# Performance work log

Measured on AMD Instinct MI355X. Metric: run time of the kernel, lower is better.

## Reference

```python
import jax, jax.numpy as jnp
import numpy as np

TEMPERATURE = 2.0 / 3.0
LIMIT_A = -0.1
LIMIT_B = 1.1

N_NODES = 50000
N_CLUSTERS = 64
N_RELATIONS = 8
N_EDGES = 1000000


def setup_inputs() -> dict:
    key = jax.random.key(0)
    ks = jax.random.split(key, 6)
    xavier = float(np.sqrt(6.0 / (N_CLUSTERS + N_CLUSTERS)))
    return {
        "assignments": jax.random.normal(ks[0], (N_NODES, N_CLUSTERS), jnp.float32),
        "inter_cluster_logits": jax.random.uniform(ks[1], (N_RELATIONS, N_CLUSTERS, N_CLUSTERS), jnp.float32, -xavier, xavier),
        "log_alpha": jnp.zeros((N_RELATIONS, N_CLUSTERS, N_CLUSTERS), jnp.float32),
        "absent_bias": jnp.zeros((N_RELATIONS,), jnp.float32),
        "edge_index": jax.random.randint(ks[2], (2, N_EDGES), 0, N_NODES, jnp.int32),
        "edge_type": jax.random.randint(ks[3], (N_EDGES,), 0, N_RELATIONS, jnp.int32),
        "neg_edge_index": jax.random.randint(ks[4], (2, N_EDGES), 0, N_NODES, jnp.int32),
        "neg_edge_type": jax.random.randint(ks[5], (N_EDGES,), 0, N_RELATIONS, jnp.int32),
    }


def _edge_logits(assignments, weights, absent_bias, edge_index, edge_type):
    # src, dst: [E, C] gathers (irregular access)
    src = assignments[edge_index[0]]
    dst = assignments[edge_index[1]]
    n_rel = weights.shape[0]
    # torch.bmm(W[et], dst[:, :, None]) == dst @ W[et].T ; compute per relation
    # (fixed small relation loop; avoids materializing [E, C, C]) then select.
    logits_all = jnp.stack(
        [jnp.sum(src * (dst @ weights[r].T), axis=-1) for r in range(n_rel)],
        axis=-1,
    )  # [E, R]
    logits = jnp.take_along_axis(logits_all, edge_type[:, None], axis=1)[:, 0]
    return logits + absent_bias[edge_type]


def reference(assignments, inter_cluster_logits, log_alpha, absent_bias,
              edge_index, edge_type, neg_edge_index, neg_edge_type):
    # Hard-concrete gate, eval mode: z = clamp(sigmoid(log_alpha)*(b-a)+a, 0, 1)
    gate = jnp.clip(jax.nn.sigmoid(log_alpha) * (LIMIT_B - LIMIT_A) + LIMIT_A, 0.0, 1.0)
    weights = jax.nn.sigmoid(inter_cluster_logits) * gate  # [R, C, C]

    pos_logits = _edge_logits(assignments, weights, absent_bias, edge_index, edge_type)
    neg_logits = _edge_logits(assignments, weights, absent_bias, neg_edge_index, neg_edge_type)

    # BCE-with-logits: target=1 -> softplus(-x); target=0 -> softplus(x)
    pos_loss = jnp.mean(jax.nn.softplus(-pos_logits))
    neg_loss = jnp.mean(jax.nn.softplus(neg_logits))
    return pos_loss + neg_loss
```

## Files before the change

kernel.cpp:

```cpp
#include <hip/hip_runtime.h>
#include <hip/hip_bf16.h>
#include <math.h>

#define E_EDGES 1000000
#define N_NODES 50000
#define N_C     64
#define N_REL   8
#define CHB     2048
#define CAP     384
#define NBLK    489
#define BT      512

typedef __attribute__((ext_vector_type(4))) float floatx4;
typedef __attribute__((ext_vector_type(2))) float floatx2;

static __device__ __forceinline__ unsigned pk4_fp8(float a, float b, float c, float d) {
    unsigned w = 0;
    w = __builtin_amdgcn_cvt_pk_fp8_f32(a, b, w, false);
    w = __builtin_amdgcn_cvt_pk_fp8_f32(c, d, w, true);
    return w;
}

static __device__ __forceinline__ long long pack64(unsigned lo, unsigned hi) {
    uint2 u; u.x = lo; u.y = hi;
    return __builtin_bit_cast(long long, u);
}

__global__ __launch_bounds__(256) void prep_kernel(
    const float* __restrict__ assign,
    const float* __restrict__ icl,
    const float* __restrict__ la,
    unsigned char* __restrict__ Wp8,
    unsigned char* __restrict__ AS8,
    float* __restrict__ out)
{
    int tid = blockIdx.x * blockDim.x + threadIdx.x;
    int nth = gridDim.x * blockDim.x;
    if (tid == 0) out[0] = 0.0f;

    for (int idx = tid; idx < N_REL * N_C * 16; idx += nth) {
        int row = idx >> 4, dq = idx & 15;
        int q = dq >> 2, c = (dq >> 1) & 1, jh = dq & 1;
        int k0 = (2 * c + jh) * 16 + 4 * q;
        float wv[4];
        #pragma unroll
        for (int b = 0; b < 4; ++b) {
            int srci = (row << 6) + k0 + b;
            float w = 1.0f / (1.0f + __expf(-icl[srci]));
            float g = 1.0f / (1.0f + __expf(-la[srci])) * 1.2f - 0.1f;
            g = fminf(fmaxf(g, 0.0f), 1.0f);
            wv[b] = w * g;
        }
        ((unsigned*)Wp8)[idx] = pk4_fp8(wv[0], wv[1], wv[2], wv[3]);
    }

    for (int n = tid; n < N_NODES; n += nth) {
        const float4* a4 = (const float4*)(assign + (size_t)n * N_C);
        unsigned w[16];
        #pragma unroll
        for (int i = 0; i < 16; ++i) {
            float4 v = a4[i];
            w[i] = pk4_fp8(v.x, v.y, v.z, v.w);
        }
        uint4* as = (uint4*)(AS8 + (size_t)n * N_C);
        #pragma unroll
        for (int q = 0; q < 4; ++q) {
            uint4 o;
            o.x = w[0 * 4 + q];
            o.y = w[1 * 4 + q];
            o.z = w[2 * 4 + q];
            o.w = w[3 * 4 + q];
            as[q] = o;
        }
    }
}

__global__ __launch_bounds__(BT, 6) void edge_kernel(
    const unsigned char* __restrict__ AS8,
    const unsigned char* __restrict__ Wp8,
    const float* __restrict__ absent_bias,
    const int* __restrict__ ei, const int* __restrict__ et,
    const int* __restrict__ nei, const int* __restrict__ net,
    float* __restrict__ out)
{
    __shared__ unsigned list[N_REL * CAP];
    __shared__ unsigned cnt[N_REL];
    __shared__ float red[8];
    if (threadIdx.x < N_REL) cnt[threadIdx.x] = 0u;
    __syncthreads();

    int blk = blockIdx.x;
    bool isneg = blk >= NBLK;
    int lb = isneg ? blk - NBLK : blk;
    const int* Es = isneg ? nei : ei;
    const int* Et = isneg ? net : et;
    float sign = isneg ? 1.0f : -1.0f;
    int base = lb * CHB;
    int elim = min(base + CHB, E_EDGES);

    for (int e = base + threadIdx.x; e < elim; e += BT) {
        int s = Es[e];
        int d = Es[E_EDGES + e];
        int r = Et[e];
        unsigned rank = atomicAdd(&cnt[r], 1u);
        if (rank < CAP) list[r * CAP + rank] = (unsigned)s | ((unsigned)d << 16);
    }
    __syncthreads();

    int lane = threadIdx.x & 63;
    int wid  = threadIdx.x >> 6;
    int n16  = lane & 15;
    int quad = lane >> 4;
    float loss = 0.0f;

    for (int r = 0; r < N_REL; ++r) {
        int n_r = min((int)cnt[r], CAP);
        if (n_r == 0) continue;
        float bias = absent_bias[r];
        uint4 wfm[4];
        #pragma unroll
        for (int mt = 0; mt < 4; ++mt)
            wfm[mt] = *(const uint4*)(Wp8 + ((r * 64 + mt * 16 + n16) << 6) + quad * 16);

        int g = wid;
        bool valid = false;
        uint4 S = {0, 0, 0, 0}, D = {0, 0, 0, 0};
        if (g * 16 < n_r) {
            int idx = g * 16 + n16;
            valid = idx < n_r;
            unsigned rec = list[r * CAP + (valid ? idx : 0)];
            S = *(const uint4*)(AS8 + ((size_t)(rec & 0xFFFF) << 6) + quad * 16);
            D = *(const uint4*)(AS8 + ((size_t)(rec >> 16) << 6) + quad * 16);
        }
        while (g * 16 < n_r) {
            int g2 = g + 8;
            bool valid2 = false;
            uint4 S2 = {0, 0, 0, 0}, D2 = {0, 0, 0, 0};
            if (g2 * 16 < n_r) {
                int idx2 = g2 * 16 + n16;
                valid2 = idx2 < n_r;
                unsigned rec2 = list[r * CAP + (valid2 ? idx2 : 0)];
                S2 = *(const uint4*)(AS8 + ((size_t)(rec2 & 0xFFFF) << 6) + quad * 16);
                D2 = *(const uint4*)(AS8 + ((size_t)(rec2 >> 16) << 6) + quad * 16);
            }

            long long bD0 = pack64(D.x, D.y);
            long long bD1 = pack64(D.z, D.w);
            floatx4 ac[4];
            #pragma unroll
            for (int mt = 0; mt < 4; ++mt) {
                floatx4 z = {0.0f, 0.0f, 0.0f, 0.0f};
                z = __builtin_amdgcn_mfma_f32_16x16x32_fp8_fp8(
                        pack64(wfm[mt].x, wfm[mt].y), bD0, z, 0, 0, 0);
                ac[mt] = __builtin_amdgcn_mfma_f32_16x16x32_fp8_fp8(
                        pack64(wfm[mt].z, wfm[mt].w), bD1, z, 0, 0, 0);
            }
            unsigned sw[4] = {S.x, S.y, S.z, S.w};
            float d0 = 0.0f, d1 = 0.0f;
            #pragma unroll
            for (int mt = 0; mt < 4; mt += 2) {
                floatx2 lo0 = __builtin_amdgcn_cvt_pk_f32_fp8((int)sw[mt], false);
                floatx2 hi0 = __builtin_amdgcn_cvt_pk_f32_fp8((int)sw[mt], true);
                floatx2 lo1 = __builtin_amdgcn_cvt_pk_f32_fp8((int)sw[mt + 1], false);
                floatx2 hi1 = __builtin_amdgcn_cvt_pk_f32_fp8((int)sw[mt + 1], true);
                d0 = fmaf(lo0.x, ac[mt][0], d0);
                d1 = fmaf(lo1.x, ac[mt + 1][0], d1);
                d0 = fmaf(lo0.y, ac[mt][1], d0);
                d1 = fmaf(lo1.y, ac[mt + 1][1], d1);
                d0 = fmaf(hi0.x, ac[mt][2], d0);
                d1 = fmaf(hi1.x, ac[mt + 1][2], d1);
                d0 = fmaf(hi0.y, ac[mt][3], d0);
                d1 = fmaf(hi1.y, ac[mt + 1][3], d1);
            }
            float dot = d0 + d1;
            dot += __shfl_xor(dot, 16);
            dot += __shfl_xor(dot, 32);
            if (quad == 0 && valid) {
                float x = sign * (dot + bias);
                loss += fmaxf(x, 0.0f) + __logf(1.0f + __expf(-fabsf(x)));
            }

            g = g2; valid = valid2; S = S2; D = D2;
        }
    }

    loss += __shfl_xor(loss, 1);
    loss += __shfl_xor(loss, 2);
    loss += __shfl_xor(loss, 4);
    loss += __shfl_xor(loss, 8);
    loss += __shfl_xor(loss, 16);
    loss += __shfl_xor(loss, 32);
    if (lane == 0) red[wid] = loss;
    __syncthreads();
    if (threadIdx.x == 0) {
        float t = red[0] + red[1] + red[2] + red[3]
                + red[4] + red[5] + red[6] + red[7];
        atomicAdd(out, t * (1.0f / (float)E_EDGES));
    }
}

extern "C" void kernel_launch(void* const* d_in, const int* in_sizes, int n_in,
                              void* d_out, int out_size, void* d_ws, size_t ws_size,
                              hipStream_t stream) {
    const float* assign = (const float*)d_in[0];
    const float* icl    = (const float*)d_in[1];
    const float* la     = (const float*)d_in[2];
    const float* ab     = (const float*)d_in[3];
    const int*   ei     = (const int*)d_in[4];
    const int*   et     = (const int*)d_in[5];
    const int*   nei    = (const int*)d_in[6];
    const int*   net    = (const int*)d_in[7];
    float* out = (float*)d_out;

    char* basep = (char*)d_ws;
    unsigned char* Wp8 = (unsigned char*)basep;
    unsigned char* AS8 = (unsigned char*)(basep + 65536);

    prep_kernel<<<256, 256, 0, stream>>>(assign, icl, la, Wp8, AS8, out);
    edge_kernel<<<2 * NBLK, BT, 0, stream>>>(AS8, Wp8, ab, ei, et, nei, net, out);
}
```

Measured before the change: 130.9 us.

## Gather edge node rows into LDS asynchronously over a flattened group list

Edge groups from all relations are flattened into one shared list so each wave handles pairs of 16-edge groups regardless of relation. Source and destination fp8 node rows are now fetched with global_load_lds 16-byte async copies into a per-wave LDS staging buffer, replacing the register-level software prefetch. Weight fragments are reloaded per group instead of held per relation, and CAP is reduced to save LDS. The aim is to balance work across waves and cut register pressure. In exchange it waits on all loads before computing, which gives up the previous overlap, and the 32KB staging buffer may limit how many blocks fit per CU.

```diff
diff --git a/kernel.cpp b/kernel.cpp
--- a/kernel.cpp
+++ b/kernel.cpp
@@ -7,7 +7,7 @@
 #define N_C     64
 #define N_REL   8
 #define CHB     2048
-#define CAP     384
+#define CAP     352
 #define NBLK    489
 #define BT      512
 
@@ -24,6 +24,15 @@
 static __device__ __forceinline__ long long pack64(unsigned lo, unsigned hi) {
     uint2 u; u.x = lo; u.y = hi;
     return __builtin_bit_cast(long long, u);
+}
+
+static __device__ __forceinline__ void async_gather16(
+    const unsigned char* gp, unsigned char* lds_base)
+{
+    __builtin_amdgcn_global_load_lds(
+        (const __attribute__((address_space(1))) void*)gp,
+        (__attribute__((address_space(3))) void*)lds_base,
+        16, 0, 0);
 }
 
 __global__ __launch_bounds__(256) void prep_kernel(
@@ -84,7 +93,10 @@
     float* __restrict__ out)
 {
     __shared__ unsigned list[N_REL * CAP];
+    __shared__ __align__(16) unsigned char stage[8][4096];
+    __shared__ unsigned glist[192];
     __shared__ unsigned cnt[N_REL];
+    __shared__ int ng_s;
     __shared__ float red[8];
     if (threadIdx.x < N_REL) cnt[threadIdx.x] = 0u;
     __syncthreads();
@@ -107,53 +119,64 @@
     }
     __syncthreads();
 
+    if (threadIdx.x == 0) {
+        int t = 0;
+        for (int r = 0; r < N_REL; ++r) {
+            int nr = min((int)cnt[r], CAP);
+            for (int b = 0; b < nr; b += 16)
+                glist[t++] = ((unsigned)r << 20) | ((unsigned)b << 8)
+                           | (unsigned)min(16, nr - b);
+        }
+        ng_s = t;
+    }
+    __syncthreads();
+    int ng = ng_s;
+
     int lane = threadIdx.x & 63;
     int wid  = threadIdx.x >> 6;
     int n16  = lane & 15;
     int quad = lane >> 4;
+    unsigned char* st = stage[wid];
     float loss = 0.0f;
 
-    for (int r = 0; r < N_REL; ++r) {
-        int n_r = min((int)cnt[r], CAP);
-        if (n_r == 0) continue;
-        float bias = absent_bias[r];
-        uint4 wfm[4];
-        #pragma unroll
-        for (int mt = 0; mt < 4; ++mt)
-            wfm[mt] = *(const uint4*)(Wp8 + ((r * 64 + mt * 16 + n16) << 6) + quad * 16);
-
-        int g = wid;
-        bool valid = false;
-        uint4 S = {0, 0, 0, 0}, D = {0, 0, 0, 0};
-        if (g * 16 < n_r) {
-            int idx = g * 16 + n16;
-            valid = idx < n_r;
-            unsigned rec = list[r * CAP + (valid ? idx : 0)];
-            S = *(const uint4*)(AS8 + ((size_t)(rec & 0xFFFF) << 6) + quad * 16);
-            D = *(const uint4*)(AS8 + ((size_t)(rec >> 16) << 6) + quad * 16);
-        }
-        while (g * 16 < n_r) {
-            int g2 = g + 8;
-            bool valid2 = false;
-            uint4 S2 = {0, 0, 0, 0}, D2 = {0, 0, 0, 0};
-            if (g2 * 16 < n_r) {
-                int idx2 = g2 * 16 + n16;
-                valid2 = idx2 < n_r;
-                unsigned rec2 = list[r * CAP + (valid2 ? idx2 : 0)];
-                S2 = *(const uint4*)(AS8 + ((size_t)(rec2 & 0xFFFF) << 6) + quad * 16);
-                D2 = *(const uint4*)(AS8 + ((size_t)(rec2 >> 16) << 6) + quad * 16);
-            }
-
+    for (int g0 = wid * 2; g0 < ng; g0 += 16) {
+        unsigned e0 = glist[g0];
+        int r0 = e0 >> 20, b0 = (e0 >> 8) & 0xFFF, c0 = e0 & 0xFF;
+        unsigned rec0 = list[r0 * CAP + b0 + min(n16, c0 - 1)];
+        async_gather16(AS8 + ((size_t)(rec0 & 0xFFFFu) << 6) + quad * 16, st);
+        async_gather16(AS8 + ((size_t)(rec0 >> 16) << 6) + quad * 16, st + 1024);
+
+        bool has1 = (g0 + 1) < ng;
+        int r1 = 0, c1 = 0;
+        if (has1) {
+            unsigned e1 = glist[g0 + 1];
+            r1 = e1 >> 20; c1 = e1 & 0xFF;
+            int b1 = (e1 >> 8) & 0xFFF;
+            unsigned rec1 = list[r1 * CAP + b1 + min(n16, c1 - 1)];
+            async_gather16(AS8 + ((size_t)(rec1 & 0xFFFFu) << 6) + quad * 16, st + 2048);
+            async_gather16(AS8 + ((size_t)(rec1 >> 16) << 6) + quad * 16, st + 3072);
+        }
+        __asm__ volatile("s_waitcnt vmcnt(0)" ::: "memory");
+
+        #pragma unroll
+        for (int h = 0; h < 2; ++h) {
+            if (h == 1 && !has1) break;
+            int r = (h == 0) ? r0 : r1;
+            int c = (h == 0) ? c0 : c1;
+            const unsigned char* sb = st + h * 2048;
+            uint4 S = *(const uint4*)(sb + lane * 16);
+            uint4 D = *(const uint4*)(sb + 1024 + lane * 16);
             long long bD0 = pack64(D.x, D.y);
             long long bD1 = pack64(D.z, D.w);
             floatx4 ac[4];
             #pragma unroll
             for (int mt = 0; mt < 4; ++mt) {
+                uint4 wf = *(const uint4*)(Wp8 + ((r * 64 + mt * 16 + n16) << 6) + quad * 16);
                 floatx4 z = {0.0f, 0.0f, 0.0f, 0.0f};
                 z = __builtin_amdgcn_mfma_f32_16x16x32_fp8_fp8(
-                        pack64(wfm[mt].x, wfm[mt].y), bD0, z, 0, 0, 0);
+                        pack64(wf.x, wf.y), bD0, z, 0, 0, 0);
                 ac[mt] = __builtin_amdgcn_mfma_f32_16x16x32_fp8_fp8(
-                        pack64(wfm[mt].z, wfm[mt].w), bD1, z, 0, 0, 0);
+                        pack64(wf.z, wf.w), bD1, z, 0, 0, 0);
             }
             unsigned sw[4] = {S.x, S.y, S.z, S.w};
             float d0 = 0.0f, d1 = 0.0f;
@@ -175,12 +198,10 @@
             float dot = d0 + d1;
             dot += __shfl_xor(dot, 16);
             dot += __shfl_xor(dot, 32);
-            if (quad == 0 && valid) {
-                float x = sign * (dot + bias);
+            if (quad == 0 && n16 < c) {
+                float x = sign * (dot + absent_bias[r]);
                 loss += fmaxf(x, 0.0f) + __logf(1.0f + __expf(-fabsf(x)));
             }
-
-            g = g2; valid = valid2; S = S2; D = D2;
         }
     }
 
```

After: 167.4 us. +27.9%, slower.
